# Performance work log

Hardware: AMD Instinct MI355X
Metric: run time of the kernel (lower is better)

The kernel has to match this reference:

```python
import jax, jax.numpy as jnp
import numpy as np

D_ENC = 512
D_DEC = 512
JOINT = 512
VOCAB = 1024


def setup_inputs() -> dict:
    key = jax.random.key(0)
    ks = jax.random.split(key, 7)
    B, T, U = 4, 256, 64
    s_enc = 1.0 / np.sqrt(D_ENC)
    s_dec = 1.0 / np.sqrt(D_DEC)
    s_out = 1.0 / np.sqrt(JOINT)
    return {
        "encoder_out": jax.random.normal(ks[0], (B, T, 1, D_ENC), dtype=jnp.float32),
        "decoder_out": jax.random.normal(ks[1], (B, 1, U, D_DEC), dtype=jnp.float32),
        # torch.nn.Linear stores weight as (out, in); uniform(-1/sqrt(in), 1/sqrt(in))
        "W_enc": jax.random.uniform(ks[2], (JOINT, D_ENC), jnp.float32, -s_enc, s_enc),
        "b_enc": jax.random.uniform(ks[3], (JOINT,), jnp.float32, -s_enc, s_enc),
        "W_dec": jax.random.uniform(ks[4], (JOINT, D_DEC), jnp.float32, -s_dec, s_dec),
        "W_out": jax.random.uniform(ks[5], (VOCAB, JOINT), jnp.float32, -s_out, s_out),
        "b_out": jax.random.uniform(ks[6], (VOCAB,), jnp.float32, -s_out, s_out),
    }


def reference(encoder_out, decoder_out, W_enc, b_enc, W_dec, W_out, b_out):
    # Project each side in its small shape first (B,T,1,J) and (B,1,U,J),
    # then broadcast-add over (T,U), tanh, output GEMM -> (B,T,U,V).
    enc = jnp.einsum("btud,jd->btuj", encoder_out, W_enc) + b_enc  # (B,T,1,J)
    dec = jnp.einsum("btud,jd->btuj", decoder_out, W_dec)          # (B,1,U,J)
    h = jnp.tanh(enc + dec)                                        # (B,T,U,J)
    return jnp.einsum("btuj,vj->btuv", h, W_out) + b_out           # (B,T,U,V)
```

## Files before the change

### kernel.cpp

```cpp
#include <hip/hip_runtime.h>
#include <hip/hip_bf16.h>


typedef __attribute__((ext_vector_type(8))) short short8;
typedef __attribute__((ext_vector_type(4))) float f32x4;

#define SZ0 524288
#define SZ1 131072
#define SZ2 262144
#define SZ3 512
#define SZ4 262144
#define SZ5 524288
#define SZ6 1024
#define CU0 0
#define CU1 524288
#define CU2 655360
#define CU3 917504
#define CU4 918016
#define CU5 1180160
#define CU6 1704448
#define CTOT 1705472

__global__ void detect_kernel(const void* p0, const void* p1, const void* p2,
                              const void* p3, const void* p4, const void* p5,
                              const void* p6, int* flags) {
  const void* ps[7] = {p0, p1, p2, p3, p4, p5, p6};
  const int sz[7] = {SZ0, SZ1, SZ2, SZ3, SZ4, SZ5, SZ6};
  const int w = threadIdx.x >> 6;
  const int l = threadIdx.x & 63;
  if (w >= 7) return;
  const unsigned short* u = (const unsigned short*)ps[w];
  const int lim = sz[w] < 1024 ? sz[w] : 1024;
  int bad = 0;
  for (int j = l; j < lim; j += 64) {
    const unsigned e = (u[j] >> 7) & 0xFFu;
    if (e >= 0x8Eu) bad = 1;
  }
  const unsigned long long b = __ballot(bad);
  if (l == 0) flags[w] = (b != 0ULL) ? 1 : 0;
}

__global__ __launch_bounds__(256) void convert_kernel(
    const void* p0, const void* p1, const void* p2, const void* p3,
    const void* p4, const void* p5, const void* p6,
    const int* __restrict__ flags, __hip_bfloat16* __restrict__ dst) {
  const int gid = blockIdx.x * 256 + threadIdx.x;
  if (gid >= CTOT) return;
  int t, local;
  const void* p;
  if (gid < CU1)      { t = 0; local = gid - CU0; p = p0; }
  else if (gid < CU2) { t = 1; local = gid - CU1; p = p1; }
  else if (gid < CU3) { t = 2; local = gid - CU2; p = p2; }
  else if (gid < CU4) { t = 3; local = gid - CU3; p = p3; }
  else if (gid < CU5) { t = 4; local = gid - CU4; p = p4; }
  else if (gid < CU6) { t = 5; local = gid - CU5; p = p5; }
  else                { t = 6; local = gid - CU6; p = p6; }
  __hip_bfloat16 v;
  if (flags[t])
    v = __float2bfloat16(((const float*)p)[local]);
  else
    v = ((const __hip_bfloat16*)p)[local];
  dst[gid] = v;
}

__device__ __forceinline__ void gemm_bt_body(
    const __hip_bfloat16* __restrict__ A, const __hip_bfloat16* __restrict__ Bw,
    const __hip_bfloat16* __restrict__ bias, float* __restrict__ C,
    int M, int N, int K, int bid,
    __hip_bfloat16* sA, __hip_bfloat16* sB) {
  const int tid = threadIdx.x;
  const int w = tid >> 6;
  const int l = tid & 63;
  const int ntiles = N >> 7;
  const int mt = bid / ntiles;
  const int nt = bid % ntiles;
  const int m0 = mt << 7;
  const int n0 = nt << 7;
  const int wm = (w >> 1) << 6;
  const int wn = (w & 1) << 6;
  const int r16 = l & 15;
  const int q = l >> 4;

  f32x4 acc[4][4] = {};

  const int srow_in = l >> 3;
  const int scol = (l & 7) << 3;

  for (int k0 = 0; k0 < K; k0 += 64) {
#pragma unroll
    for (int i = 0; i < 4; ++i) {
      const int c = (w << 2) + i;
      const int row = (c << 3) + srow_in;
      const __hip_bfloat16* gA = A + (size_t)(m0 + row) * K + k0 + scol;
      const __hip_bfloat16* gB = Bw + (size_t)(n0 + row) * K + k0 + scol;
      __builtin_amdgcn_global_load_lds(
          (const __attribute__((address_space(1))) void*)gA,
          (__attribute__((address_space(3))) void*)(sA + (c << 9) + (l << 3)),
          16, 0, 0);
      __builtin_amdgcn_global_load_lds(
          (const __attribute__((address_space(1))) void*)gB,
          (__attribute__((address_space(3))) void*)(sB + (c << 9) + (l << 3)),
          16, 0, 0);
    }
    __syncthreads();

#pragma unroll
    for (int kk = 0; kk < 2; ++kk) {
      const int kc = (kk << 5) + (q << 3);
      short8 af[4], bf[4];
#pragma unroll
      for (int mi = 0; mi < 4; ++mi)
        af[mi] = *(const short8*)(sA + (wm + (mi << 4) + r16) * 64 + kc);
#pragma unroll
      for (int ni = 0; ni < 4; ++ni)
        bf[ni] = *(const short8*)(sB + (wn + (ni << 4) + r16) * 64 + kc);
#pragma unroll
      for (int mi = 0; mi < 4; ++mi)
#pragma unroll
        for (int ni = 0; ni < 4; ++ni)
          acc[mi][ni] = __builtin_amdgcn_mfma_f32_16x16x32_bf16(
              af[mi], bf[ni], acc[mi][ni], 0, 0, 0);
    }
    __syncthreads();
  }

#pragma unroll
  for (int ni = 0; ni < 4; ++ni) {
    const int col = n0 + wn + (ni << 4) + r16;
    const float bc = bias ? __bfloat162float(bias[col]) : 0.0f;
#pragma unroll
    for (int mi = 0; mi < 4; ++mi) {
      const int rowb = m0 + wm + (mi << 4) + (q << 2);
#pragma unroll
      for (int i = 0; i < 4; ++i)
        C[(size_t)(rowb + i) * N + col] = acc[mi][ni][i] + bc;
    }
  }
}

__global__ __launch_bounds__(256) void proj_kernel(
    const __hip_bfloat16* __restrict__ enc, const __hip_bfloat16* __restrict__ Wenc,
    const __hip_bfloat16* __restrict__ benc,
    const __hip_bfloat16* __restrict__ dec, const __hip_bfloat16* __restrict__ Wdec,
    float* __restrict__ Pe, float* __restrict__ Pd) {
  __shared__ __align__(16) __hip_bfloat16 sA[128 * 64];
  __shared__ __align__(16) __hip_bfloat16 sB[128 * 64];
  if (blockIdx.x < 32)
    gemm_bt_body(enc, Wenc, benc, Pe, 1024, 512, 512, blockIdx.x, sA, sB);
  else
    gemm_bt_body(dec, Wdec, nullptr, Pd, 256, 512, 512, blockIdx.x - 32, sA, sB);
}

__global__ __launch_bounds__(512, 4) void gemm_joint(
    const float* __restrict__ Pe, const float* __restrict__ Pd,
    const __hip_bfloat16* __restrict__ Bw,
    const __hip_bfloat16* __restrict__ bias, float* __restrict__ out) {
  __shared__ __align__(16) __hip_bfloat16 sH[64 * 512];
  __shared__ __align__(16) __hip_bfloat16 sB[2][128 * 32];

  const int t = threadIdx.x;
  const int w = t >> 6;
  const int l = t & 63;
  const int r16 = l & 15;
  const int q = l >> 4;
  const int m0 = blockIdx.x << 6;

  auto stage = [&](int iter, int buf) {
    const int n0 = (iter >> 4) << 7;
    const int k0 = (iter & 15) << 5;
    const int row = t >> 2;
    const int cc = t & 3;
    const int s = (row & 3) ^ ((row >> 2) & 3);
    const __hip_bfloat16* src =
        Bw + (size_t)(n0 + row) * 512 + k0 + ((cc ^ s) << 3);
    __builtin_amdgcn_global_load_lds(
        (const __attribute__((address_space(1))) void*)src,
        (__attribute__((address_space(3))) void*)(&sB[buf][0] + (t << 3)),
        16, 0, 0);
  };

  stage(0, 0);

  {
    const int r = t & 63;
    const int seg = t >> 6;
    const int e = blockIdx.x;
    const int d = ((blockIdx.x >> 8) << 6) | r;
    const float* pe = Pe + (size_t)e * 512 + (seg << 6);
    const float* pd = Pd + (size_t)d * 512 + (seg << 6);
#pragma unroll
    for (int i = 0; i < 8; ++i) {
      const int cc = (seg << 3) + i;
      const f32x4 a0 = *(const f32x4*)(pe + (i << 3));
      const f32x4 a1 = *(const f32x4*)(pe + (i << 3) + 4);
      const f32x4 b0 = *(const f32x4*)(pd + (i << 3));
      const f32x4 b1 = *(const f32x4*)(pd + (i << 3) + 4);
      short8 hv;
#pragma unroll
      for (int jj = 0; jj < 4; ++jj) {
        float s = a0[jj] + b0[jj];
        float tv = 1.0f - 2.0f / (__expf(2.0f * s) + 1.0f);
        __hip_bfloat16 hb = __float2bfloat16(tv);
        hv[jj] = *(const short*)&hb;
        s = a1[jj] + b1[jj];
        tv = 1.0f - 2.0f / (__expf(2.0f * s) + 1.0f);
        hb = __float2bfloat16(tv);
        hv[4 + jj] = *(const short*)&hb;
      }
      *(short8*)(sH + (r << 9) + ((cc ^ (r & 7)) << 3)) = hv;
    }
  }
  __syncthreads();

  const int wm = (w >> 2) << 5;
  const int wn = (w & 3) << 5;
  f32x4 acc[2][2] = {};

  int aoff[2], boff[2];
#pragma unroll
  for (int mi = 0; mi < 2; ++mi) aoff[mi] = (wm + (mi << 4) + r16) << 9;
#pragma unroll
  for (int ni = 0; ni < 2; ++ni) {
    const int row = wn + (ni << 4) + r16;
    const int s = (row & 3) ^ ((row >> 2) & 3);
    boff[ni] = (row << 5) + ((q ^ s) << 3);
  }
  const int swzA = r16 & 7;

  int buf = 0;
  for (int iter = 0; iter < 128; ++iter) {
    if (iter < 127) stage(iter + 1, buf ^ 1);

    const int cbase = (iter & 15) << 2;
    const int ch = ((cbase + q) ^ swzA) << 3;
    short8 af[2], bf[2];
#pragma unroll
    for (int mi = 0; mi < 2; ++mi)
      af[mi] = *(const short8*)(sH + aoff[mi] + ch);
#pragma unroll
    for (int ni = 0; ni < 2; ++ni)
      bf[ni] = *(const short8*)(&sB[buf][0] + boff[ni]);
#pragma unroll
    for (int mi = 0; mi < 2; ++mi)
#pragma unroll
      for (int ni = 0; ni < 2; ++ni)
        acc[mi][ni] = __builtin_amdgcn_mfma_f32_16x16x32_bf16(
            af[mi], bf[ni], acc[mi][ni], 0, 0, 0);

    if ((iter & 15) == 15) {
      const int n0 = (iter >> 4) << 7;
#pragma unroll
      for (int ni = 0; ni < 2; ++ni) {
        const int col = n0 + wn + (ni << 4) + r16;
        const float bc = __bfloat162float(bias[col]);
#pragma unroll
        for (int mi = 0; mi < 2; ++mi) {
          const int rowb = m0 + wm + (mi << 4) + (q << 2);
#pragma unroll
          for (int i = 0; i < 4; ++i)
            out[(size_t)(rowb + i) * 1024 + col] = acc[mi][ni][i] + bc;
        }
      }
#pragma unroll
      for (int mi = 0; mi < 2; ++mi)
#pragma unroll
        for (int ni = 0; ni < 2; ++ni)
          acc[mi][ni] = (f32x4){0.0f, 0.0f, 0.0f, 0.0f};
    }

    __syncthreads();
    buf ^= 1;
  }
}

extern "C" void kernel_launch(void* const* d_in, const int* in_sizes, int n_in,
                              void* d_out, int out_size, void* d_ws,
                              size_t ws_size, hipStream_t stream) {
  char* ws = (char*)d_ws;
  int* flags = (int*)ws;
  __hip_bfloat16* cp = (__hip_bfloat16*)(ws + 256);
  float* Pe = (float*)(ws + (4ull << 20));
  float* Pd = (float*)(ws + (6ull << 20));

  detect_kernel<<<dim3(1), dim3(512), 0, stream>>>(
      d_in[0], d_in[1], d_in[2], d_in[3], d_in[4], d_in[5], d_in[6], flags);
  convert_kernel<<<dim3((CTOT + 255) / 256), dim3(256), 0, stream>>>(
      d_in[0], d_in[1], d_in[2], d_in[3], d_in[4], d_in[5], d_in[6], flags, cp);

  const __hip_bfloat16* enc_c = cp + CU0;
  const __hip_bfloat16* dec_c = cp + CU1;
  const __hip_bfloat16* Wenc_c = cp + CU2;
  const __hip_bfloat16* benc_c = cp + CU3;
  const __hip_bfloat16* Wdec_c = cp + CU4;
  const __hip_bfloat16* Wout_c = cp + CU5;
  const __hip_bfloat16* bout_c = cp + CU6;

  proj_kernel<<<dim3(40), dim3(256), 0, stream>>>(enc_c, Wenc_c, benc_c,
                                                  dec_c, Wdec_c, Pe, Pd);
  gemm_joint<<<dim3(1024), dim3(512), 0, stream>>>(
      Pe, Pd, Wout_c, bout_c, (float*)d_out);
}
```

Baseline: 402.1 us.

## Switch joint GEMM to 32x32 MFMA with direct global weight loads, no B LDS staging

The joint output GEMM no longer stages W_out tiles through double-buffered shared memory with per-iteration barriers. Each wave now loads its weight fragments straight from global memory into registers, prefetching two k-steps ahead, and uses 32x32x16 MFMA with a 32x64 per-wave tile over four 256-column passes. The LDS swizzle for the tanh activations changes to fit the new read pattern. This removes barrier and LDS traffic for B, at the cost of more global/L2 weight reads per block and higher register pressure.

```diff
diff --git a/kernel.cpp b/kernel.cpp
--- a/kernel.cpp
+++ b/kernel.cpp
@@ -4,6 +4,7 @@
 
 typedef __attribute__((ext_vector_type(8))) short short8;
 typedef __attribute__((ext_vector_type(4))) float f32x4;
+typedef __attribute__((ext_vector_type(16))) float f32x16;
 
 #define SZ0 524288
 #define SZ1 131072
@@ -156,30 +157,13 @@
     const __hip_bfloat16* __restrict__ Bw,
     const __hip_bfloat16* __restrict__ bias, float* __restrict__ out) {
   __shared__ __align__(16) __hip_bfloat16 sH[64 * 512];
-  __shared__ __align__(16) __hip_bfloat16 sB[2][128 * 32];
 
   const int t = threadIdx.x;
   const int w = t >> 6;
   const int l = t & 63;
-  const int r16 = l & 15;
-  const int q = l >> 4;
+  const int l31 = l & 31;
+  const int q2 = l >> 5;
   const int m0 = blockIdx.x << 6;
-
-  auto stage = [&](int iter, int buf) {
-    const int n0 = (iter >> 4) << 7;
-    const int k0 = (iter & 15) << 5;
-    const int row = t >> 2;
-    const int cc = t & 3;
-    const int s = (row & 3) ^ ((row >> 2) & 3);
-    const __hip_bfloat16* src =
-        Bw + (size_t)(n0 + row) * 512 + k0 + ((cc ^ s) << 3);
-    __builtin_amdgcn_global_load_lds(
-        (const __attribute__((address_space(1))) void*)src,
-        (__attribute__((address_space(3))) void*)(&sB[buf][0] + (t << 3)),
-        16, 0, 0);
-  };
-
-  stage(0, 0);
 
   {
     const int r = t & 63;
@@ -188,6 +172,7 @@
     const int d = ((blockIdx.x >> 8) << 6) | r;
     const float* pe = Pe + (size_t)e * 512 + (seg << 6);
     const float* pd = Pd + (size_t)d * 512 + (seg << 6);
+    const int swr = (r & 7) ^ (((r >> 3) & 1) << 3);
 #pragma unroll
     for (int i = 0; i < 8; ++i) {
       const int cc = (seg << 3) + i;
@@ -207,69 +192,54 @@
         hb = __float2bfloat16(tv);
         hv[4 + jj] = *(const short*)&hb;
       }
-      *(short8*)(sH + (r << 9) + ((cc ^ (r & 7)) << 3)) = hv;
+      *(short8*)(sH + (r << 9) + ((cc ^ swr) << 3)) = hv;
     }
   }
   __syncthreads();
 
-  const int wm = (w >> 2) << 5;
-  const int wn = (w & 3) << 5;
-  f32x4 acc[2][2] = {};
-
-  int aoff[2], boff[2];
-#pragma unroll
-  for (int mi = 0; mi < 2; ++mi) aoff[mi] = (wm + (mi << 4) + r16) << 9;
-#pragma unroll
-  for (int ni = 0; ni < 2; ++ni) {
-    const int row = wn + (ni << 4) + r16;
-    const int s = (row & 3) ^ ((row >> 2) & 3);
-    boff[ni] = (row << 5) + ((q ^ s) << 3);
-  }
-  const int swzA = r16 & 7;
-
-  int buf = 0;
-  for (int iter = 0; iter < 128; ++iter) {
-    if (iter < 127) stage(iter + 1, buf ^ 1);
-
-    const int cbase = (iter & 15) << 2;
-    const int ch = ((cbase + q) ^ swzA) << 3;
-    short8 af[2], bf[2];
-#pragma unroll
-    for (int mi = 0; mi < 2; ++mi)
-      af[mi] = *(const short8*)(sH + aoff[mi] + ch);
-#pragma unroll
-    for (int ni = 0; ni < 2; ++ni)
-      bf[ni] = *(const short8*)(&sB[buf][0] + boff[ni]);
-#pragma unroll
-    for (int mi = 0; mi < 2; ++mi)
-#pragma unroll
-      for (int ni = 0; ni < 2; ++ni)
-        acc[mi][ni] = __builtin_amdgcn_mfma_f32_16x16x32_bf16(
-            af[mi], bf[ni], acc[mi][ni], 0, 0, 0);
-
-    if ((iter & 15) == 15) {
-      const int n0 = (iter >> 4) << 7;
-#pragma unroll
-      for (int ni = 0; ni < 2; ++ni) {
-        const int col = n0 + wn + (ni << 4) + r16;
-        const float bc = __bfloat162float(bias[col]);
-#pragma unroll
-        for (int mi = 0; mi < 2; ++mi) {
-          const int rowb = m0 + wm + (mi << 4) + (q << 2);
-#pragma unroll
-          for (int i = 0; i < 4; ++i)
-            out[(size_t)(rowb + i) * 1024 + col] = acc[mi][ni][i] + bc;
-        }
-      }
-#pragma unroll
-      for (int mi = 0; mi < 2; ++mi)
-#pragma unroll
-        for (int ni = 0; ni < 2; ++ni)
-          acc[mi][ni] = (f32x4){0.0f, 0.0f, 0.0f, 0.0f};
-    }
-
-    __syncthreads();
-    buf ^= 1;
+  const int wm = (w & 1) << 5;
+  const int wn = (w >> 1) << 6;
+  const int aoff = (wm + l31) << 9;
+  const int swz = (l & 7) ^ (((l >> 3) & 1) << 3);
+
+  for (int nt = 0; nt < 4; ++nt) {
+    const int n0 = nt << 8;
+    const __hip_bfloat16* bp0 = Bw + (size_t)(n0 + wn + l31) * 512 + (q2 << 3);
+    const __hip_bfloat16* bp1 = bp0 + (32 * 512);
+    short8 c0 = *(const short8*)(bp0);
+    short8 c1 = *(const short8*)(bp1);
+    short8 d0 = *(const short8*)(bp0 + 16);
+    short8 d1 = *(const short8*)(bp1 + 16);
+    f32x16 acc0 = {};
+    f32x16 acc1 = {};
+#pragma unroll 4
+    for (int kp = 0; kp < 16; ++kp) {
+      const int ks0 = kp << 1;
+      const int ks1 = ks0 + 1;
+      const short8 p0a = *(const short8*)(bp0 + (((ks0 + 2) & 31) << 4));
+      const short8 p0b = *(const short8*)(bp1 + (((ks0 + 2) & 31) << 4));
+      const short8 p1a = *(const short8*)(bp0 + (((ks1 + 2) & 31) << 4));
+      const short8 p1b = *(const short8*)(bp1 + (((ks1 + 2) & 31) << 4));
+      const short8 afA =
+          *(const short8*)(sH + aoff + ((((ks0 << 1) + q2) ^ swz) << 3));
+      acc0 = __builtin_amdgcn_mfma_f32_32x32x16_bf16(afA, c0, acc0, 0, 0, 0);
+      acc1 = __builtin_amdgcn_mfma_f32_32x32x16_bf16(afA, c1, acc1, 0, 0, 0);
+      const short8 afB =
+          *(const short8*)(sH + aoff + ((((ks1 << 1) + q2) ^ swz) << 3));
+      acc0 = __builtin_amdgcn_mfma_f32_32x32x16_bf16(afB, d0, acc0, 0, 0, 0);
+      acc1 = __builtin_amdgcn_mfma_f32_32x32x16_bf16(afB, d1, acc1, 0, 0, 0);
+      c0 = p0a; c1 = p0b; d0 = p1a; d1 = p1b;
+    }
+
+    const int colb = n0 + wn + l31;
+    const float bc0 = __bfloat162float(bias[colb]);
+    const float bc1 = __bfloat162float(bias[colb + 32]);
+#pragma unroll
+    for (int r = 0; r < 16; ++r) {
+      const int row = m0 + wm + (r & 3) + ((r >> 2) << 3) + (q2 << 2);
+      out[(size_t)row * 1024 + colb] = acc0[r] + bc0;
+      out[(size_t)row * 1024 + colb + 32] = acc1[r] + bc1;
+    }
   }
 }
 
```

Result: slower. 517.4 us (+28.7%).

## Enlarge joint GEMM tiles to 128 rows with 32x32x16 MFMA and 1024-thread blocks

Applied to the files above, without the earlier changes.

Each joint-GEMM block now builds 128 rows of tanh activations (two encoder frames) in LDS and runs 16 waves. Each wave computes a 64x64 output tile with 32x32x16 bf16 MFMA instructions, and the B tile grows to 512 columns by 16 K per stage. The aim is more reuse of each staged W_out slice and fewer LDS reads per MFMA, which should cut global and LDS traffic per output. In exchange the block doubles LDS use to about 160KB, which limits residency to one block per CU. The B staging in LDS also drops its swizzle, which risks bank conflicts.

```diff
diff --git a/kernel.cpp b/kernel.cpp
--- a/kernel.cpp
+++ b/kernel.cpp
@@ -4,6 +4,7 @@
 
 typedef __attribute__((ext_vector_type(8))) short short8;
 typedef __attribute__((ext_vector_type(4))) float f32x4;
+typedef __attribute__((ext_vector_type(16))) float f32x16;
 
 #define SZ0 524288
 #define SZ1 131072
@@ -151,43 +152,42 @@
     gemm_bt_body(dec, Wdec, nullptr, Pd, 256, 512, 512, blockIdx.x - 32, sA, sB);
 }
 
-__global__ __launch_bounds__(512, 4) void gemm_joint(
+__global__ __launch_bounds__(1024, 4) void gemm_joint(
     const float* __restrict__ Pe, const float* __restrict__ Pd,
     const __hip_bfloat16* __restrict__ Bw,
     const __hip_bfloat16* __restrict__ bias, float* __restrict__ out) {
-  __shared__ __align__(16) __hip_bfloat16 sH[64 * 512];
-  __shared__ __align__(16) __hip_bfloat16 sB[2][128 * 32];
+  __shared__ __align__(16) __hip_bfloat16 sH[128 * 512];
+  __shared__ __align__(16) __hip_bfloat16 sB[2 * 8192];
 
   const int t = threadIdx.x;
   const int w = t >> 6;
   const int l = t & 63;
-  const int r16 = l & 15;
-  const int q = l >> 4;
-  const int m0 = blockIdx.x << 6;
+  const int l31 = l & 31;
+  const int q2 = l >> 5;
+  const int m0 = blockIdx.x << 7;
 
   auto stage = [&](int iter, int buf) {
-    const int n0 = (iter >> 4) << 7;
-    const int k0 = (iter & 15) << 5;
-    const int row = t >> 2;
-    const int cc = t & 3;
-    const int s = (row & 3) ^ ((row >> 2) & 3);
-    const __hip_bfloat16* src =
-        Bw + (size_t)(n0 + row) * 512 + k0 + ((cc ^ s) << 3);
+    const int n0 = (iter >> 5) << 9;
+    const int k0 = (iter & 31) << 4;
+    const int n = t & 511;
+    const int c = t >> 9;
+    const __hip_bfloat16* src = Bw + (size_t)(n0 + n) * 512 + k0 + (c << 3);
     __builtin_amdgcn_global_load_lds(
         (const __attribute__((address_space(1))) void*)src,
-        (__attribute__((address_space(3))) void*)(&sB[buf][0] + (t << 3)),
+        (__attribute__((address_space(3))) void*)(sB + (buf << 13) + (t << 3)),
         16, 0, 0);
   };
 
   stage(0, 0);
 
   {
-    const int r = t & 63;
-    const int seg = t >> 6;
-    const int e = blockIdx.x;
-    const int d = ((blockIdx.x >> 8) << 6) | r;
+    const int r = t & 127;
+    const int seg = t >> 7;
+    const int e = (blockIdx.x << 1) + (r >> 6);
+    const int d = ((blockIdx.x >> 7) << 6) | (r & 63);
     const float* pe = Pe + (size_t)e * 512 + (seg << 6);
     const float* pd = Pd + (size_t)d * 512 + (seg << 6);
+    const int swr = r & 63;
 #pragma unroll
     for (int i = 0; i < 8; ++i) {
       const int cc = (seg << 3) + i;
@@ -207,65 +207,63 @@
         hb = __float2bfloat16(tv);
         hv[4 + jj] = *(const short*)&hb;
       }
-      *(short8*)(sH + (r << 9) + ((cc ^ (r & 7)) << 3)) = hv;
+      *(short8*)(sH + (r << 9) + ((cc ^ swr) << 3)) = hv;
     }
   }
   __syncthreads();
 
-  const int wm = (w >> 2) << 5;
-  const int wn = (w & 3) << 5;
-  f32x4 acc[2][2] = {};
-
-  int aoff[2], boff[2];
-#pragma unroll
-  for (int mi = 0; mi < 2; ++mi) aoff[mi] = (wm + (mi << 4) + r16) << 9;
-#pragma unroll
-  for (int ni = 0; ni < 2; ++ni) {
-    const int row = wn + (ni << 4) + r16;
-    const int s = (row & 3) ^ ((row >> 2) & 3);
-    boff[ni] = (row << 5) + ((q ^ s) << 3);
-  }
-  const int swzA = r16 & 7;
+  const int wm = (w >> 3) << 6;
+  const int wn = (w & 7) << 6;
+  f32x16 acc[2][2] = {};
+
+  int arow[2], aswz[2];
+#pragma unroll
+  for (int mi = 0; mi < 2; ++mi) {
+    const int row = wm + (mi << 5) + l31;
+    arow[mi] = row << 9;
+    aswz[mi] = row & 63;
+  }
+  int boff[2];
+#pragma unroll
+  for (int ni = 0; ni < 2; ++ni)
+    boff[ni] = (q2 << 12) + ((wn + (ni << 5) + l31) << 3);
 
   int buf = 0;
-  for (int iter = 0; iter < 128; ++iter) {
-    if (iter < 127) stage(iter + 1, buf ^ 1);
-
-    const int cbase = (iter & 15) << 2;
-    const int ch = ((cbase + q) ^ swzA) << 3;
+  for (int iter = 0; iter < 64; ++iter) {
+    if (iter < 63) stage(iter + 1, buf ^ 1);
+
+    const int cb = ((iter & 31) << 1) + q2;
     short8 af[2], bf[2];
 #pragma unroll
     for (int mi = 0; mi < 2; ++mi)
-      af[mi] = *(const short8*)(sH + aoff[mi] + ch);
+      af[mi] = *(const short8*)(sH + arow[mi] + ((cb ^ aswz[mi]) << 3));
 #pragma unroll
     for (int ni = 0; ni < 2; ++ni)
-      bf[ni] = *(const short8*)(&sB[buf][0] + boff[ni]);
+      bf[ni] = *(const short8*)(sB + (buf << 13) + boff[ni]);
 #pragma unroll
     for (int mi = 0; mi < 2; ++mi)
 #pragma unroll
       for (int ni = 0; ni < 2; ++ni)
-        acc[mi][ni] = __builtin_amdgcn_mfma_f32_16x16x32_bf16(
+        acc[mi][ni] = __builtin_amdgcn_mfma_f32_32x32x16_bf16(
             af[mi], bf[ni], acc[mi][ni], 0, 0, 0);
 
-    if ((iter & 15) == 15) {
-      const int n0 = (iter >> 4) << 7;
+    if ((iter & 31) == 31) {
+      const int n0 = (iter >> 5) << 9;
 #pragma unroll
       for (int ni = 0; ni < 2; ++ni) {
-        const int col = n0 + wn + (ni << 4) + r16;
+        const int col = n0 + wn + (ni << 5) + l31;
         const float bc = __bfloat162float(bias[col]);
 #pragma unroll
         for (int mi = 0; mi < 2; ++mi) {
-          const int rowb = m0 + wm + (mi << 4) + (q << 2);
-#pragma unroll
-          for (int i = 0; i < 4; ++i)
-            out[(size_t)(rowb + i) * 1024 + col] = acc[mi][ni][i] + bc;
+#pragma unroll
+          for (int rr = 0; rr < 16; ++rr) {
+            const int row = m0 + wm + (mi << 5) + (rr & 3) + ((rr >> 2) << 3) +
+                            (q2 << 2);
+            out[(size_t)row * 1024 + col] = acc[mi][ni][rr] + bc;
+          }
+          acc[mi][ni] = (f32x16){};
         }
       }
-#pragma unroll
-      for (int mi = 0; mi < 2; ++mi)
-#pragma unroll
-        for (int ni = 0; ni < 2; ++ni)
-          acc[mi][ni] = (f32x4){0.0f, 0.0f, 0.0f, 0.0f};
     }
 
     __syncthreads();
@@ -297,6 +295,6 @@
 
   proj_kernel<<<dim3(40), dim3(256), 0, stream>>>(enc_c, Wenc_c, benc_c,
                                                   dec_c, Wdec_c, Pe, Pd);
-  gemm_joint<<<dim3(1024), dim3(512), 0, stream>>>(
+  gemm_joint<<<dim3(512), dim3(1024), 0, stream>>>(
       Pe, Pd, Wout_c, bout_c, (float*)d_out);
 }
```

New measurement: 482.4 us. +20.0%, slower.
